# Optimization experiments

Hardware: AMD Instinct MI355X
Metric: run time of the kernel (lower is better)

Reference implementation:

```python
import jax, jax.numpy as jnp
import numpy as np

DIM = 1536
NUM_HEADS = 12
HEAD_DIM = DIM // NUM_HEADS  # 128
EPS = 1e-6


def _rms_norm(x, weight, eps=EPS):
    # x: [B, S, C], computed in float32 like the torch module
    xf = x.astype(jnp.float32)
    xf = xf * jax.lax.rsqrt(jnp.mean(xf * xf, axis=-1, keepdims=True) + eps)
    return (xf * weight).astype(x.dtype)


def _rotate_half(x):
    x1, x2 = jnp.split(x, 2, axis=-1)
    return jnp.concatenate([-x2, x1], axis=-1)


def setup_inputs() -> dict:
    key = jax.random.key(0)
    ks = jax.random.split(key, 12)
    B, S = 1, 4096
    scale = 1.0 / np.sqrt(DIM)
    x = jax.random.normal(ks[0], (B, S, DIM), dtype=jnp.float32)
    # RoPE tables [S, head_dim]
    pos = jnp.arange(S, dtype=jnp.float32)[:, None]
    inv_freq = 1.0 / (10000.0 ** (jnp.arange(0, HEAD_DIM, 2, dtype=jnp.float32) / HEAD_DIM))
    ang = pos * inv_freq[None, :]                      # [S, head_dim/2]
    ang = jnp.concatenate([ang, ang], axis=-1)         # [S, head_dim]
    freqs_cos = jnp.cos(ang)
    freqs_sin = jnp.sin(ang)
    Wq = jax.random.normal(ks[1], (DIM, DIM), dtype=jnp.float32) * scale
    bq = jnp.zeros((DIM,), dtype=jnp.float32)
    Wk = jax.random.normal(ks[2], (DIM, DIM), dtype=jnp.float32) * scale
    bk = jnp.zeros((DIM,), dtype=jnp.float32)
    Wv = jax.random.normal(ks[3], (DIM, DIM), dtype=jnp.float32) * scale
    bv = jnp.zeros((DIM,), dtype=jnp.float32)
    Wo = jax.random.normal(ks[4], (DIM, DIM), dtype=jnp.float32) * scale
    bo = jnp.zeros((DIM,), dtype=jnp.float32)
    gq = jnp.ones((DIM,), dtype=jnp.float32)
    gk = jnp.ones((DIM,), dtype=jnp.float32)
    return {"x": x, "freqs_cos": freqs_cos, "freqs_sin": freqs_sin,
            "Wq": Wq, "bq": bq, "Wk": Wk, "bk": bk, "Wv": Wv, "bv": bv,
            "Wo": Wo, "bo": bo, "gq": gq, "gk": gk}


def reference(x, freqs_cos, freqs_sin, Wq, bq, Wk, bk, Wv, bv, Wo, bo, gq, gk):
    b, s, _ = x.shape
    n, d = NUM_HEADS, HEAD_DIM
    q = _rms_norm(x @ Wq.T + bq, gq).reshape(b, s, n, d)
    k = _rms_norm(x @ Wk.T + bk, gk).reshape(b, s, n, d)
    v = (x @ Wv.T + bv).reshape(b, s, n, d)
    # RoPE: freqs [S, d] -> broadcast over batch and heads
    cos = freqs_cos[None, :, None, :]
    sin = freqs_sin[None, :, None, :]
    q = q * cos + _rotate_half(q) * sin
    k = k * cos + _rotate_half(k) * sin
    # SDPA, non-causal
    scores = jnp.einsum('bqnd,bknd->bnqk', q, k) / jnp.sqrt(jnp.asarray(d, x.dtype))
    attn = jax.nn.softmax(scores, axis=-1)
    out = jnp.einsum('bnqk,bknd->bqnd', attn, v).reshape(b, s, n * d)
    return out @ Wo.T + bo
```

## Files before the change

### kernel.cpp

```cpp
#include <hip/hip_runtime.h>

typedef unsigned short ushort_t;
typedef short bf16x8 __attribute__((ext_vector_type(8)));
typedef float f32x4 __attribute__((ext_vector_type(4)));
typedef float f32x16 __attribute__((ext_vector_type(16)));

#define S_LEN 4096
#define DIM   1536
#define NH    12
#define HD    128
#define KVSPLIT 4
#define ROWS (NH * S_LEN)
#define OPSPLIT_ELEMS ((size_t)ROWS * HD)

__device__ __forceinline__ float bf2f(ushort_t h) {
  union { unsigned u; float f; } v; v.u = ((unsigned)h) << 16; return v.f;
}
__device__ __forceinline__ ushort_t f2bf(float f) {
  union { float f; unsigned u; } v; v.f = f;
  return (ushort_t)((v.u + 0x7FFFu + ((v.u >> 16) & 1u)) >> 16);
}
__device__ __forceinline__ unsigned cvtpk(float lo, float hi_) {
  unsigned r; asm("v_cvt_pk_bf16_f32 %0, %1, %2" : "=v"(r) : "v"(lo), "v"(hi_)); return r;
}

#define GLD16(gp, lp) __builtin_amdgcn_global_load_lds( \
    (const __attribute__((address_space(1))) unsigned int*)(gp), \
    (__attribute__((address_space(3))) unsigned int*)(lp), 16, 0, 0)

__global__ void __launch_bounds__(256) cvt_bf16(const float* __restrict__ in,
                                                ushort_t* __restrict__ out, int n4) {
  int i = blockIdx.x * 256 + threadIdx.x;
  int stride = gridDim.x * 256;
  for (; i < n4; i += stride) {
    float4 v = ((const float4*)in)[i];
    ushort4 o;
    o.x = f2bf(v.x); o.y = f2bf(v.y); o.z = f2bf(v.z); o.w = f2bf(v.w);
    ((ushort4*)out)[i] = o;
  }
}

template <int F32OUT>
__global__ void __launch_bounds__(256) gemm_bt(
    const ushort_t* __restrict__ A, const ushort_t* __restrict__ Wbase,
    const float* __restrict__ b0, const float* __restrict__ b1, const float* __restrict__ b2,
    void* __restrict__ Cbase_v, int M, int N, int K)
{
  const int z = blockIdx.z;
  const ushort_t* W = Wbase + (size_t)z * N * K;
  const float* bias = (z == 0) ? b0 : (z == 1) ? b1 : b2;

  const int n0 = blockIdx.x * 128;
  const int m0 = blockIdx.y * 128;
  const int t = threadIdx.x;
  const int lane = t & 63;
  const int w = t >> 6;
  const int wr = w >> 1, wc = w & 1;
  const int mp = lane & 15, g = lane >> 4;

  __shared__ __attribute__((aligned(16))) ushort_t As[128 * 64];
  __shared__ __attribute__((aligned(16))) ushort_t Bs[128 * 64];

  f32x4 acc[4][4];
  f32x4 zero = {0.f, 0.f, 0.f, 0.f};
#pragma unroll
  for (int i = 0; i < 4; ++i)
#pragma unroll
    for (int j = 0; j < 4; ++j) acc[i][j] = zero;

  for (int kt = 0; kt < K; kt += 64) {
    __syncthreads();
#pragma unroll
    for (int i = 0; i < 4; ++i) {
      int p = i * 256 + t;
      int r = p >> 3, sl = p & 7;
      int sg = sl ^ (r & 7);
      GLD16(A + (size_t)(m0 + r) * K + kt + sg * 8, As + p * 8);
      GLD16(W + (size_t)(n0 + r) * K + kt + sg * 8, Bs + p * 8);
    }
    __syncthreads();
#pragma unroll
    for (int kk = 0; kk < 2; ++kk) {
      bf16x8 af[4], bfr[4];
#pragma unroll
      for (int mi = 0; mi < 4; ++mi) {
        int row = wr * 64 + mi * 16 + mp;
        int ch = (g + 4 * kk) ^ (row & 7);
        af[mi] = *(const bf16x8*)(As + row * 64 + ch * 8);
      }
#pragma unroll
      for (int ni = 0; ni < 4; ++ni) {
        int row = wc * 64 + ni * 16 + mp;
        int ch = (g + 4 * kk) ^ (row & 7);
        bfr[ni] = *(const bf16x8*)(Bs + row * 64 + ch * 8);
      }
#pragma unroll
      for (int mi = 0; mi < 4; ++mi)
#pragma unroll
        for (int ni = 0; ni < 4; ++ni)
          acc[mi][ni] = __builtin_amdgcn_mfma_f32_16x16x32_bf16(af[mi], bfr[ni], acc[mi][ni], 0, 0, 0);
    }
  }
#pragma unroll
  for (int ni = 0; ni < 4; ++ni) {
    int n = n0 + wc * 64 + ni * 16 + mp;
    float bv = bias[n];
#pragma unroll
    for (int mi = 0; mi < 4; ++mi) {
      int mbase = m0 + wr * 64 + mi * 16 + g * 4;
#pragma unroll
      for (int j = 0; j < 4; ++j) {
        if constexpr (F32OUT) {
          ((float*)Cbase_v)[(size_t)z * M * N + (size_t)(mbase + j) * N + n] =
              acc[mi][ni][j] + bv;
        } else {
          ((ushort_t*)Cbase_v)[(size_t)z * M * N + (size_t)(mbase + j) * N + n] =
              f2bf(acc[mi][ni][j] + bv);
        }
      }
    }
  }
}

__global__ void __launch_bounds__(256) epi_qkv(
    const ushort_t* __restrict__ raw,
    const float* __restrict__ gq, const float* __restrict__ gk,
    const float* __restrict__ fcos, const float* __restrict__ fsin,
    ushort_t* __restrict__ Qh, ushort_t* __restrict__ Kh, ushort_t* __restrict__ Vh)
{
  const int s = blockIdx.x;
  const int t = threadIdx.x;
  const ushort_t* rq = raw + (size_t)s * DIM;
  const ushort_t* rk = raw + (size_t)S_LEN * DIM + (size_t)s * DIM;
  const ushort_t* rv = raw + 2 * (size_t)S_LEN * DIM + (size_t)s * DIM;

  float sq = 0.f, sk = 0.f;
#pragma unroll
  for (int i = 0; i < 6; ++i) {
    int e = t + 256 * i;
    float a = bf2f(rq[e]); sq += a * a;
    float b = bf2f(rk[e]); sk += b * b;
  }
  for (int off = 1; off < 64; off <<= 1) {
    sq += __shfl_xor(sq, off, 64);
    sk += __shfl_xor(sk, off, 64);
  }
  __shared__ float red[2][4];
  int w = t >> 6;
  if ((t & 63) == 0) { red[0][w] = sq; red[1][w] = sk; }
  __syncthreads();
  sq = red[0][0] + red[0][1] + red[0][2] + red[0][3];
  sk = red[1][0] + red[1][1] + red[1][2] + red[1][3];
  float invq = rsqrtf(sq * (1.f / 1536.f) + 1e-6f);
  float invk = rsqrtf(sk * (1.f / 1536.f) + 1e-6f);

  const float qscale = 0.12752004708465604f;
#pragma unroll
  for (int i = 0; i < 3; ++i) {
    int p = t + 256 * i;
    int hh = p >> 6, d = p & 63;
    int e1 = hh * 128 + d, e2 = e1 + 64;
    float c1 = fcos[s * 128 + d],      s1 = fsin[s * 128 + d];
    float c2 = fcos[s * 128 + d + 64], s2 = fsin[s * 128 + d + 64];
    float q1 = bf2f(rq[e1]) * invq * gq[e1];
    float q2 = bf2f(rq[e2]) * invq * gq[e2];
    float k1 = bf2f(rk[e1]) * invk * gk[e1];
    float k2 = bf2f(rk[e2]) * invk * gk[e2];
    size_t ob = ((size_t)hh * S_LEN + s) * 128;
    Qh[ob + d]      = f2bf((q1 * c1 - q2 * s1) * qscale);
    Qh[ob + d + 64] = f2bf((q2 * c2 + q1 * s2) * qscale);
    Kh[ob + d]      = f2bf(k1 * c1 - k2 * s1);
    Kh[ob + d + 64] = f2bf(k2 * c2 + k1 * s2);
  }
#pragma unroll
  for (int i = 0; i < 6; ++i) {
    int e = t + 256 * i;
    int hh = e >> 7, d = e & 127;
    Vh[((size_t)hh * S_LEN + s) * 128 + d] = rv[e];
  }
}

__global__ void __launch_bounds__(256) transpose_v(const ushort_t* __restrict__ Vh,
                                                   ushort_t* __restrict__ VT) {
  const int st = blockIdx.x * 64;
  const int dt = blockIdx.y * 64;
  const int h = blockIdx.z;
  __shared__ ushort_t tile[64][65];
  const int t = threadIdx.x;
#pragma unroll
  for (int i = 0; i < 2; ++i) {
    int p = i * 256 + t;
    int r = p >> 3, c = (p & 7) * 8;
    bf16x8 v = *(const bf16x8*)(Vh + ((size_t)h * S_LEN + st + r) * 128 + dt + c);
#pragma unroll
    for (int j = 0; j < 8; ++j) tile[r][c + j] = ((ushort_t*)&v)[j];
  }
  __syncthreads();
#pragma unroll
  for (int i = 0; i < 2; ++i) {
    int p = i * 256 + t;
    int r = p >> 3, c = (p & 7) * 8;
    ushort_t tmp[8];
#pragma unroll
    for (int j = 0; j < 8; ++j) tmp[j] = tile[c + j][r];
    *(bf16x8*)(VT + ((size_t)h * 128 + dt + r) * S_LEN + st + c) = *(bf16x8*)tmp;
  }
}

__global__ void __launch_bounds__(128) attn32(
    const ushort_t* __restrict__ Qh, const ushort_t* __restrict__ Kh,
    const ushort_t* __restrict__ VT,
    ushort_t* __restrict__ opraw, ushort_t* __restrict__ opxb,
    float* __restrict__ mlbuf)
{
  const int qt = blockIdx.x;
  const int h = blockIdx.y;
  const int z = blockIdx.z;
  const int t = threadIdx.x;
  const int lane = t & 63;
  const int w = t >> 6;
  const int ql = lane & 31;
  const int hi = lane >> 5;

  __shared__ __attribute__((aligned(16))) ushort_t Ks[64 * 128];
  __shared__ __attribute__((aligned(16))) ushort_t Vs[128 * 64];

  const int q0 = qt * 64 + w * 32;
  const size_t kbase = (size_t)h * S_LEN * 128;
  const size_t vbase = (size_t)h * 128 * S_LEN;

  bf16x8 qf[8];
#pragma unroll
  for (int s = 0; s < 8; ++s)
    qf[s] = *(const bf16x8*)(Qh + ((size_t)h * S_LEN + q0 + ql) * 128 + 16 * s + 8 * hi);

  f32x16 oacc[4];
#pragma unroll
  for (int dt = 0; dt < 4; ++dt)
#pragma unroll
    for (int r = 0; r < 16; ++r) oacc[dt][r] = 0.f;
  float mrun = -1e30f, lrun = 0.f;

  const int kvbeg = z * (S_LEN / KVSPLIT);
  const int kvend = kvbeg + S_LEN / KVSPLIT;
  for (int kv0 = kvbeg; kv0 < kvend; kv0 += 64) {
    __syncthreads();
#pragma unroll
    for (int i = 0; i < 8; ++i) {
      int p = i * 128 + t;
      int r = p >> 4, sl = p & 15;
      int sg = sl ^ (r & 7);
      GLD16(Kh + kbase + (size_t)(kv0 + r) * 128 + sg * 8, Ks + p * 8);
    }
#pragma unroll
    for (int i = 0; i < 8; ++i) {
      int p = i * 128 + t;
      int r = p >> 3, sl = p & 7;
      int sg = sl ^ (r & 7);
      GLD16(VT + vbase + (size_t)r * S_LEN + kv0 + sg * 8, Vs + p * 8);
    }
    __syncthreads();

    f32x16 sa0, sa1;
#pragma unroll
    for (int r = 0; r < 16; ++r) { sa0[r] = 0.f; sa1[r] = 0.f; }
    __builtin_amdgcn_s_setprio(1);
#pragma unroll
    for (int s = 0; s < 8; ++s) {
      int ck = (2 * s + hi) ^ (ql & 7);
      bf16x8 k0 = *(const bf16x8*)(Ks + ql * 128 + ck * 8);
      bf16x8 k1 = *(const bf16x8*)(Ks + (32 + ql) * 128 + ck * 8);
      sa0 = __builtin_amdgcn_mfma_f32_32x32x16_bf16(k0, qf[s], sa0, 0, 0, 0);
      sa1 = __builtin_amdgcn_mfma_f32_32x32x16_bf16(k1, qf[s], sa1, 0, 0, 0);
    }
    __builtin_amdgcn_s_setprio(0);

    float mt[8];
#pragma unroll
    for (int r = 0; r < 8; ++r)
      mt[r] = fmaxf(fmaxf(sa0[r], sa0[r + 8]), fmaxf(sa1[r], sa1[r + 8]));
#pragma unroll
    for (int off = 4; off > 0; off >>= 1)
#pragma unroll
      for (int r = 0; r < 8; ++r)
        if (r < off) mt[r] = fmaxf(mt[r], mt[r + off]);
    float mx = fmaxf(mt[0], __shfl_xor(mt[0], 32));

    if (__any(mx - mrun > 11.0f)) {
      float nm = fmaxf(mrun, mx);
      float sc = exp2f(mrun - nm);
      mrun = nm;
      lrun *= sc;
#pragma unroll
      for (int dt = 0; dt < 4; ++dt)
#pragma unroll
        for (int r = 0; r < 16; ++r) oacc[dt][r] *= sc;
    }

    float rt[8];
#pragma unroll
    for (int r = 0; r < 16; ++r) {
      sa0[r] = exp2f(sa0[r] - mrun);
      sa1[r] = exp2f(sa1[r] - mrun);
    }
#pragma unroll
    for (int r = 0; r < 8; ++r) rt[r] = (sa0[r] + sa0[r + 8]) + (sa1[r] + sa1[r + 8]);
#pragma unroll
    for (int off = 4; off > 0; off >>= 1)
#pragma unroll
      for (int r = 0; r < 8; ++r)
        if (r < off) rt[r] += rt[r + off];
    lrun += rt[0] + __shfl_xor(rt[0], 32);

    unsigned pw0[8], pw1[8];
#pragma unroll
    for (int a = 0; a < 4; ++a) {
      pw0[2 * a]     = cvtpk(sa0[4 * a], sa0[4 * a + 1]);
      pw0[2 * a + 1] = cvtpk(sa0[4 * a + 2], sa0[4 * a + 3]);
      pw1[2 * a]     = cvtpk(sa1[4 * a], sa1[4 * a + 1]);
      pw1[2 * a + 1] = cvtpk(sa1[4 * a + 2], sa1[4 * a + 3]);
    }

#pragma unroll
    for (int st = 0; st < 2; ++st) {
#pragma unroll
      for (int ks = 0; ks < 2; ++ks) {
        unsigned q0w0 = st ? pw1[4 * ks + 0] : pw0[4 * ks + 0];
        unsigned q0w1 = st ? pw1[4 * ks + 1] : pw0[4 * ks + 1];
        unsigned q1w0 = st ? pw1[4 * ks + 2] : pw0[4 * ks + 2];
        unsigned q1w1 = st ? pw1[4 * ks + 3] : pw0[4 * ks + 3];
        unsigned sw0 = hi ? q0w0 : q1w0;
        unsigned sw1 = hi ? q0w1 : q1w1;
        unsigned rv0 = (unsigned)__shfl_xor((int)sw0, 32);
        unsigned rv1 = (unsigned)__shfl_xor((int)sw1, 32);
        union { unsigned u[4]; bf16x8 v; } fw;
        fw.u[0] = hi ? rv0 : q0w0;
        fw.u[1] = hi ? rv1 : q0w1;
        fw.u[2] = hi ? q1w0 : rv0;
        fw.u[3] = hi ? q1w1 : rv1;
        __builtin_amdgcn_s_setprio(1);
#pragma unroll
        for (int dt = 0; dt < 4; ++dt) {
          int d = 32 * dt + ql;
          int cv = (4 * st + 2 * ks + hi) ^ (ql & 7);
          bf16x8 va = *(const bf16x8*)(Vs + d * 64 + cv * 8);
          oacc[dt] = __builtin_amdgcn_mfma_f32_32x32x16_bf16(va, fw.v, oacc[dt], 0, 0, 0);
        }
        __builtin_amdgcn_s_setprio(0);
      }
    }
  }

  ushort_t* Op = (z < 3) ? (opraw + (size_t)z * OPSPLIT_ELEMS) : opxb;
  const int row = h * S_LEN + q0 + ql;
  float inv = 1.f / lrun;
#pragma unroll
  for (int dt = 0; dt < 4; ++dt) {
#pragma unroll
    for (int c = 0; c < 4; ++c) {
      float f0 = oacc[dt][4 * c + 0] * inv, f1 = oacc[dt][4 * c + 1] * inv;
      float f2 = oacc[dt][4 * c + 2] * inv, f3 = oacc[dt][4 * c + 3] * inv;
      uint2 u;
      u.x = cvtpk(f0, f1);
      u.y = cvtpk(f2, f3);
      *(uint2*)(Op + (size_t)row * 128 + 32 * dt + 8 * c + 4 * hi) = u;
    }
  }
  if (hi == 0) {
    mlbuf[2 * ((size_t)z * ROWS + row)]     = mrun;
    mlbuf[2 * ((size_t)z * ROWS + row) + 1] = lrun;
  }
}

__global__ void __launch_bounds__(256) attn_combine(
    const ushort_t* __restrict__ opraw, const ushort_t* __restrict__ opxb,
    const float* __restrict__ mlbuf, ushort_t* __restrict__ hb)
{
  int gidx = blockIdx.x * 256 + threadIdx.x;
  int r = gidx >> 4;
  int c = gidx & 15;

  float m[KVSPLIT], l[KVSPLIT];
#pragma unroll
  for (int zz = 0; zz < KVSPLIT; ++zz) {
    m[zz] = mlbuf[2 * ((size_t)zz * ROWS + r)];
    l[zz] = mlbuf[2 * ((size_t)zz * ROWS + r) + 1];
  }
  float M = fmaxf(fmaxf(m[0], m[1]), fmaxf(m[2], m[3]));
  float wsum = 0.f, wz[KVSPLIT];
#pragma unroll
  for (int zz = 0; zz < KVSPLIT; ++zz) {
    wz[zz] = l[zz] * exp2f(m[zz] - M);
    wsum += wz[zz];
  }
  float invw = 1.f / wsum;

  float o[8];
#pragma unroll
  for (int j = 0; j < 8; ++j) o[j] = 0.f;
#pragma unroll
  for (int zz = 0; zz < KVSPLIT; ++zz) {
    const ushort_t* Op = (zz < 3) ? (opraw + (size_t)zz * OPSPLIT_ELEMS) : opxb;
    bf16x8 v = *(const bf16x8*)(Op + (size_t)r * 128 + c * 8);
#pragma unroll
    for (int j = 0; j < 8; ++j) o[j] += wz[zz] * bf2f((ushort_t)v[j]);
  }
  uint4 u;
  u.x = cvtpk(o[0] * invw, o[1] * invw);
  u.y = cvtpk(o[2] * invw, o[3] * invw);
  u.z = cvtpk(o[4] * invw, o[5] * invw);
  u.w = cvtpk(o[6] * invw, o[7] * invw);
  int q = r & (S_LEN - 1), h = r >> 12;
  *(uint4*)(hb + (size_t)q * DIM + h * 128 + c * 8) = u;
}

extern "C" void kernel_launch(void* const* d_in, const int* in_sizes, int n_in,
                              void* d_out, int out_size, void* d_ws, size_t ws_size,
                              hipStream_t stream) {
  const float* x    = (const float*)d_in[0];
  const float* fcos = (const float*)d_in[1];
  const float* fsin = (const float*)d_in[2];
  const float* Wq   = (const float*)d_in[3];
  const float* bq   = (const float*)d_in[4];
  const float* Wk   = (const float*)d_in[5];
  const float* bk   = (const float*)d_in[6];
  const float* Wv   = (const float*)d_in[7];
  const float* bv   = (const float*)d_in[8];
  const float* Wo   = (const float*)d_in[9];
  const float* bo   = (const float*)d_in[10];
  const float* gq   = (const float*)d_in[11];
  const float* gk   = (const float*)d_in[12];

  char* ws = (char*)d_ws;
  ushort_t* xb  = (ushort_t*)(ws);
  ushort_t* wb  = (ushort_t*)(ws + 12582912);
  ushort_t* raw = (ushort_t*)(ws + 31457280);
  ushort_t* Qh  = (ushort_t*)(ws + 69206016);
  ushort_t* Kh  = (ushort_t*)(ws + 81788928);
  ushort_t* Vh  = (ushort_t*)(ws + 94371840);
  ushort_t* VT  = (ushort_t*)(ws + 106954752);
  ushort_t* hb  = (ushort_t*)(ws + 119537664);

  cvt_bf16<<<2048, 256, 0, stream>>>(x,  xb,             6291456 / 4);
  cvt_bf16<<<2048, 256, 0, stream>>>(Wq, wb + 0 * 2359296, 2359296 / 4);
  cvt_bf16<<<2048, 256, 0, stream>>>(Wk, wb + 1 * 2359296, 2359296 / 4);
  cvt_bf16<<<2048, 256, 0, stream>>>(Wv, wb + 2 * 2359296, 2359296 / 4);
  cvt_bf16<<<2048, 256, 0, stream>>>(Wo, wb + 3 * 2359296, 2359296 / 4);

  gemm_bt<0><<<dim3(12, 32, 3), 256, 0, stream>>>(xb, wb, bq, bk, bv,
                                                  (void*)raw, 4096, 1536, 1536);
  epi_qkv<<<4096, 256, 0, stream>>>(raw, gq, gk, fcos, fsin, Qh, Kh, Vh);
  transpose_v<<<dim3(64, 2, 12), 256, 0, stream>>>(Vh, VT);
  attn32<<<dim3(64, 12, KVSPLIT), 128, 0, stream>>>(Qh, Kh, VT, raw, xb, (float*)Vh);
  attn_combine<<<3072, 256, 0, stream>>>(raw, xb, (const float*)Vh, hb);
  gemm_bt<1><<<dim3(12, 32, 1), 256, 0, stream>>>(hb, wb + 3 * 2359296, bo, bo, bo,
                                                  (void*)d_out, 4096, 1536, 1536);
}
```

Measured before the change: 529.7 us.

## Add double-buffered KV staging attention kernel for half the KV splits

```diff
diff --git a/kernel.cpp b/kernel.cpp
--- a/kernel.cpp
+++ b/kernel.cpp
@@ -207,15 +207,156 @@
   }
 }
 
+__device__ __forceinline__ void stage_kv(const ushort_t* __restrict__ Kg,
+                                         const ushort_t* __restrict__ Vg,
+                                         ushort_t* KsB, ushort_t* VsB, int t) {
+#pragma unroll
+  for (int i = 0; i < 8; ++i) {
+    int p = i * 128 + t;
+    int r = p >> 4, sl = p & 15;
+    int sg = sl ^ (r & 7);
+    GLD16(Kg + (size_t)r * 128 + sg * 8, KsB + p * 8);
+  }
+#pragma unroll
+  for (int i = 0; i < 8; ++i) {
+    int p = i * 128 + t;
+    int r = p >> 3, sl = p & 7;
+    int sg = sl ^ (r & 7);
+    GLD16(Vg + (size_t)r * S_LEN + sg * 8, VsB + p * 8);
+  }
+}
+
+struct AttnState {
+  f32x16 oacc[4];
+  float mrun, lrun;
+};
+
+__device__ __forceinline__ void attn_tile(const ushort_t* KsB, const ushort_t* VsB,
+                                          const bf16x8* qf, AttnState& st_,
+                                          int ql, int hi) {
+  f32x16 sa0, sa1;
+#pragma unroll
+  for (int r = 0; r < 16; ++r) { sa0[r] = 0.f; sa1[r] = 0.f; }
+  __builtin_amdgcn_s_setprio(1);
+#pragma unroll
+  for (int s = 0; s < 8; ++s) {
+    int ck = (2 * s + hi) ^ (ql & 7);
+    bf16x8 k0 = *(const bf16x8*)(KsB + ql * 128 + ck * 8);
+    bf16x8 k1 = *(const bf16x8*)(KsB + (32 + ql) * 128 + ck * 8);
+    sa0 = __builtin_amdgcn_mfma_f32_32x32x16_bf16(k0, qf[s], sa0, 0, 0, 0);
+    sa1 = __builtin_amdgcn_mfma_f32_32x32x16_bf16(k1, qf[s], sa1, 0, 0, 0);
+  }
+  __builtin_amdgcn_s_setprio(0);
+
+  float mt[8];
+#pragma unroll
+  for (int r = 0; r < 8; ++r)
+    mt[r] = fmaxf(fmaxf(sa0[r], sa0[r + 8]), fmaxf(sa1[r], sa1[r + 8]));
+#pragma unroll
+  for (int off = 4; off > 0; off >>= 1)
+#pragma unroll
+    for (int r = 0; r < 8; ++r)
+      if (r < off) mt[r] = fmaxf(mt[r], mt[r + off]);
+  float mx = fmaxf(mt[0], __shfl_xor(mt[0], 32));
+
+  if (__any(mx - st_.mrun > 11.0f)) {
+    float nm = fmaxf(st_.mrun, mx);
+    float sc = exp2f(st_.mrun - nm);
+    st_.mrun = nm;
+    st_.lrun *= sc;
+#pragma unroll
+    for (int dt = 0; dt < 4; ++dt)
+#pragma unroll
+      for (int r = 0; r < 16; ++r) st_.oacc[dt][r] *= sc;
+  }
+
+  float rt[8];
+#pragma unroll
+  for (int r = 0; r < 16; ++r) {
+    sa0[r] = exp2f(sa0[r] - st_.mrun);
+    sa1[r] = exp2f(sa1[r] - st_.mrun);
+  }
+#pragma unroll
+  for (int r = 0; r < 8; ++r) rt[r] = (sa0[r] + sa0[r + 8]) + (sa1[r] + sa1[r + 8]);
+#pragma unroll
+  for (int off = 4; off > 0; off >>= 1)
+#pragma unroll
+    for (int r = 0; r < 8; ++r)
+      if (r < off) rt[r] += rt[r + off];
+  st_.lrun += rt[0] + __shfl_xor(rt[0], 32);
+
+  unsigned pw0[8], pw1[8];
+#pragma unroll
+  for (int a = 0; a < 4; ++a) {
+    pw0[2 * a]     = cvtpk(sa0[4 * a], sa0[4 * a + 1]);
+    pw0[2 * a + 1] = cvtpk(sa0[4 * a + 2], sa0[4 * a + 3]);
+    pw1[2 * a]     = cvtpk(sa1[4 * a], sa1[4 * a + 1]);
+    pw1[2 * a + 1] = cvtpk(sa1[4 * a + 2], sa1[4 * a + 3]);
+  }
+
+#pragma unroll
+  for (int sx = 0; sx < 2; ++sx) {
+#pragma unroll
+    for (int ks = 0; ks < 2; ++ks) {
+      unsigned q0w0 = sx ? pw1[4 * ks + 0] : pw0[4 * ks + 0];
+      unsigned q0w1 = sx ? pw1[4 * ks + 1] : pw0[4 * ks + 1];
+      unsigned q1w0 = sx ? pw1[4 * ks + 2] : pw0[4 * ks + 2];
+      unsigned q1w1 = sx ? pw1[4 * ks + 3] : pw0[4 * ks + 3];
+      unsigned sw0 = hi ? q0w0 : q1w0;
+      unsigned sw1 = hi ? q0w1 : q1w1;
+      unsigned rv0 = (unsigned)__shfl_xor((int)sw0, 32);
+      unsigned rv1 = (unsigned)__shfl_xor((int)sw1, 32);
+      union { unsigned u[4]; bf16x8 v; } fw;
+      fw.u[0] = hi ? rv0 : q0w0;
+      fw.u[1] = hi ? rv1 : q0w1;
+      fw.u[2] = hi ? q1w0 : rv0;
+      fw.u[3] = hi ? q1w1 : rv1;
+      __builtin_amdgcn_s_setprio(1);
+#pragma unroll
+      for (int dt = 0; dt < 4; ++dt) {
+        int d = 32 * dt + ql;
+        int cv = (4 * sx + 2 * ks + hi) ^ (ql & 7);
+        bf16x8 va = *(const bf16x8*)(VsB + d * 64 + cv * 8);
+        st_.oacc[dt] = __builtin_amdgcn_mfma_f32_32x32x16_bf16(va, fw.v, st_.oacc[dt], 0, 0, 0);
+      }
+      __builtin_amdgcn_s_setprio(0);
+    }
+  }
+}
+
+__device__ __forceinline__ void attn_epilogue(AttnState& st_, int z, int row, int hi,
+                                              ushort_t* __restrict__ opraw,
+                                              ushort_t* __restrict__ opxb,
+                                              float* __restrict__ mlbuf) {
+  ushort_t* Op = (z < 3) ? (opraw + (size_t)z * OPSPLIT_ELEMS) : opxb;
+  float inv = 1.f / st_.lrun;
+#pragma unroll
+  for (int dt = 0; dt < 4; ++dt) {
+#pragma unroll
+    for (int c = 0; c < 4; ++c) {
+      float f0 = st_.oacc[dt][4 * c + 0] * inv, f1 = st_.oacc[dt][4 * c + 1] * inv;
+      float f2 = st_.oacc[dt][4 * c + 2] * inv, f3 = st_.oacc[dt][4 * c + 3] * inv;
+      uint2 u;
+      u.x = cvtpk(f0, f1);
+      u.y = cvtpk(f2, f3);
+      *(uint2*)(Op + (size_t)row * 128 + 32 * dt + 8 * c + 4 * hi) = u;
+    }
+  }
+  if (hi == 0) {
+    mlbuf[2 * ((size_t)z * ROWS + row)]     = st_.mrun;
+    mlbuf[2 * ((size_t)z * ROWS + row) + 1] = st_.lrun;
+  }
+}
+
 __global__ void __launch_bounds__(128) attn32(
     const ushort_t* __restrict__ Qh, const ushort_t* __restrict__ Kh,
     const ushort_t* __restrict__ VT,
     ushort_t* __restrict__ opraw, ushort_t* __restrict__ opxb,
-    float* __restrict__ mlbuf)
+    float* __restrict__ mlbuf, int zoff)
 {
   const int qt = blockIdx.x;
   const int h = blockIdx.y;
-  const int z = blockIdx.z;
+  const int z = blockIdx.z + zoff;
   const int t = threadIdx.x;
   const int lane = t & 63;
   const int w = t >> 6;
@@ -234,142 +375,79 @@
   for (int s = 0; s < 8; ++s)
     qf[s] = *(const bf16x8*)(Qh + ((size_t)h * S_LEN + q0 + ql) * 128 + 16 * s + 8 * hi);
 
-  f32x16 oacc[4];
+  AttnState st_;
 #pragma unroll
   for (int dt = 0; dt < 4; ++dt)
 #pragma unroll
-    for (int r = 0; r < 16; ++r) oacc[dt][r] = 0.f;
-  float mrun = -1e30f, lrun = 0.f;
+    for (int r = 0; r < 16; ++r) st_.oacc[dt][r] = 0.f;
+  st_.mrun = -1e30f; st_.lrun = 0.f;
 
   const int kvbeg = z * (S_LEN / KVSPLIT);
   const int kvend = kvbeg + S_LEN / KVSPLIT;
   for (int kv0 = kvbeg; kv0 < kvend; kv0 += 64) {
     __syncthreads();
-#pragma unroll
-    for (int i = 0; i < 8; ++i) {
-      int p = i * 128 + t;
-      int r = p >> 4, sl = p & 15;
-      int sg = sl ^ (r & 7);
-      GLD16(Kh + kbase + (size_t)(kv0 + r) * 128 + sg * 8, Ks + p * 8);
+    stage_kv(Kh + kbase + (size_t)kv0 * 128, VT + vbase + kv0, Ks, Vs, t);
+    __syncthreads();
+    attn_tile(Ks, Vs, qf, st_, ql, hi);
+  }
+  attn_epilogue(st_, z, h * S_LEN + q0 + ql, hi, opraw, opxb, mlbuf);
+}
+
+__global__ void __launch_bounds__(128) attn32p(
+    const ushort_t* __restrict__ Qh, const ushort_t* __restrict__ Kh,
+    const ushort_t* __restrict__ VT,
+    ushort_t* __restrict__ opraw, ushort_t* __restrict__ opxb,
+    float* __restrict__ mlbuf, int zoff)
+{
+  const int qt = blockIdx.x;
+  const int h = blockIdx.y;
+  const int z = blockIdx.z + zoff;
+  const int t = threadIdx.x;
+  const int lane = t & 63;
+  const int w = t >> 6;
+  const int ql = lane & 31;
+  const int hi = lane >> 5;
+
+  __shared__ __attribute__((aligned(16))) ushort_t Ks[2][64 * 128];
+  __shared__ __attribute__((aligned(16))) ushort_t Vs[2][128 * 64];
+
+  const int q0 = qt * 64 + w * 32;
+  const size_t kbase = (size_t)h * S_LEN * 128;
+  const size_t vbase = (size_t)h * 128 * S_LEN;
+
+  bf16x8 qf[8];
+#pragma unroll
+  for (int s = 0; s < 8; ++s)
+    qf[s] = *(const bf16x8*)(Qh + ((size_t)h * S_LEN + q0 + ql) * 128 + 16 * s + 8 * hi);
+
+  AttnState st_;
+#pragma unroll
+  for (int dt = 0; dt < 4; ++dt)
+#pragma unroll
+    for (int r = 0; r < 16; ++r) st_.oacc[dt][r] = 0.f;
+  st_.mrun = -1e30f; st_.lrun = 0.f;
+
+  const int kvbeg = z * (S_LEN / KVSPLIT);
+  const int NT = (S_LEN / KVSPLIT) / 64;
+
+  stage_kv(Kh + kbase + (size_t)kvbeg * 128, VT + vbase + kvbeg, Ks[0], Vs[0], t);
+
+  for (int it = 0; it < NT; ++it) {
+    const int cur = it & 1;
+    if (it + 1 < NT) {
+      const int kvn = kvbeg + (it + 1) * 64;
+      stage_kv(Kh + kbase + (size_t)kvn * 128, VT + vbase + kvn, Ks[cur ^ 1], Vs[cur ^ 1], t);
+      asm volatile("s_waitcnt vmcnt(16)" ::: "memory");
+    } else {
+      asm volatile("s_waitcnt vmcnt(0)" ::: "memory");
     }
-#pragma unroll
-    for (int i = 0; i < 8; ++i) {
-      int p = i * 128 + t;
-      int r = p >> 3, sl = p & 7;
-      int sg = sl ^ (r & 7);
-      GLD16(VT + vbase + (size_t)r * S_LEN + kv0 + sg * 8, Vs + p * 8);
-    }
-    __syncthreads();
-
-    f32x16 sa0, sa1;
-#pragma unroll
-    for (int r = 0; r < 16; ++r) { sa0[r] = 0.f; sa1[r] = 0.f; }
-    __builtin_amdgcn_s_setprio(1);
-#pragma unroll
-    for (int s = 0; s < 8; ++s) {
-      int ck = (2 * s + hi) ^ (ql & 7);
-      bf16x8 k0 = *(const bf16x8*)(Ks + ql * 128 + ck * 8);
-      bf16x8 k1 = *(const bf16x8*)(Ks + (32 + ql) * 128 + ck * 8);
-      sa0 = __builtin_amdgcn_mfma_f32_32x32x16_bf16(k0, qf[s], sa0, 0, 0, 0);
-      sa1 = __builtin_amdgcn_mfma_f32_32x32x16_bf16(k1, qf[s], sa1, 0, 0, 0);
-    }
-    __builtin_amdgcn_s_setprio(0);
-
-    float mt[8];
-#pragma unroll
-    for (int r = 0; r < 8; ++r)
-      mt[r] = fmaxf(fmaxf(sa0[r], sa0[r + 8]), fmaxf(sa1[r], sa1[r + 8]));
-#pragma unroll
-    for (int off = 4; off > 0; off >>= 1)
-#pragma unroll
-      for (int r = 0; r < 8; ++r)
-        if (r < off) mt[r] = fmaxf(mt[r], mt[r + off]);
-    float mx = fmaxf(mt[0], __shfl_xor(mt[0], 32));
-
-    if (__any(mx - mrun > 11.0f)) {
-      float nm = fmaxf(mrun, mx);
-      float sc = exp2f(mrun - nm);
-      mrun = nm;
-      lrun *= sc;
-#pragma unroll
-      for (int dt = 0; dt < 4; ++dt)
-#pragma unroll
-        for (int r = 0; r < 16; ++r) oacc[dt][r] *= sc;
-    }
-
-    float rt[8];
-#pragma unroll
-    for (int r = 0; r < 16; ++r) {
-      sa0[r] = exp2f(sa0[r] - mrun);
-      sa1[r] = exp2f(sa1[r] - mrun);
-    }
-#pragma unroll
-    for (int r = 0; r < 8; ++r) rt[r] = (sa0[r] + sa0[r + 8]) + (sa1[r] + sa1[r + 8]);
-#pragma unroll
-    for (int off = 4; off > 0; off >>= 1)
-#pragma unroll
-      for (int r = 0; r < 8; ++r)
-        if (r < off) rt[r] += rt[r + off];
-    lrun += rt[0] + __shfl_xor(rt[0], 32);
-
-    unsigned pw0[8], pw1[8];
-#pragma unroll
-    for (int a = 0; a < 4; ++a) {
-      pw0[2 * a]     = cvtpk(sa0[4 * a], sa0[4 * a + 1]);
-      pw0[2 * a + 1] = cvtpk(sa0[4 * a + 2], sa0[4 * a + 3]);
-      pw1[2 * a]     = cvtpk(sa1[4 * a], sa1[4 * a + 1]);
-      pw1[2 * a + 1] = cvtpk(sa1[4 * a + 2], sa1[4 * a + 3]);
-    }
-
-#pragma unroll
-    for (int st = 0; st < 2; ++st) {
-#pragma unroll
-      for (int ks = 0; ks < 2; ++ks) {
-        unsigned q0w0 = st ? pw1[4 * ks + 0] : pw0[4 * ks + 0];
-        unsigned q0w1 = st ? pw1[4 * ks + 1] : pw0[4 * ks + 1];
-        unsigned q1w0 = st ? pw1[4 * ks + 2] : pw0[4 * ks + 2];
-        unsigned q1w1 = st ? pw1[4 * ks + 3] : pw0[4 * ks + 3];
-        unsigned sw0 = hi ? q0w0 : q1w0;
-        unsigned sw1 = hi ? q0w1 : q1w1;
-        unsigned rv0 = (unsigned)__shfl_xor((int)sw0, 32);
-        unsigned rv1 = (unsigned)__shfl_xor((int)sw1, 32);
-        union { unsigned u[4]; bf16x8 v; } fw;
-        fw.u[0] = hi ? rv0 : q0w0;
-        fw.u[1] = hi ? rv1 : q0w1;
-        fw.u[2] = hi ? q1w0 : rv0;
-        fw.u[3] = hi ? q1w1 : rv1;
-        __builtin_amdgcn_s_setprio(1);
-#pragma unroll
-        for (int dt = 0; dt < 4; ++dt) {
-          int d = 32 * dt + ql;
-          int cv = (4 * st + 2 * ks + hi) ^ (ql & 7);
-          bf16x8 va = *(const bf16x8*)(Vs + d * 64 + cv * 8);
-          oacc[dt] = __builtin_amdgcn_mfma_f32_32x32x16_bf16(va, fw.v, oacc[dt], 0, 0, 0);
-        }
-        __builtin_amdgcn_s_setprio(0);
-      }
-    }
-  }
-
-  ushort_t* Op = (z < 3) ? (opraw + (size_t)z * OPSPLIT_ELEMS) : opxb;
-  const int row = h * S_LEN + q0 + ql;
-  float inv = 1.f / lrun;
-#pragma unroll
-  for (int dt = 0; dt < 4; ++dt) {
-#pragma unroll
-    for (int c = 0; c < 4; ++c) {
-      float f0 = oacc[dt][4 * c + 0] * inv, f1 = oacc[dt][4 * c + 1] * inv;
-      float f2 = oacc[dt][4 * c + 2] * inv, f3 = oacc[dt][4 * c + 3] * inv;
-      uint2 u;
-      u.x = cvtpk(f0, f1);
-      u.y = cvtpk(f2, f3);
-      *(uint2*)(Op + (size_t)row * 128 + 32 * dt + 8 * c + 4 * hi) = u;
-    }
-  }
-  if (hi == 0) {
-    mlbuf[2 * ((size_t)z * ROWS + row)]     = mrun;
-    mlbuf[2 * ((size_t)z * ROWS + row) + 1] = lrun;
-  }
+    __builtin_amdgcn_sched_barrier(0);
+    __builtin_amdgcn_s_barrier();
+    __builtin_amdgcn_sched_barrier(0);
+    attn_tile(Ks[cur], Vs[cur], qf, st_, ql, hi);
+    __builtin_amdgcn_s_barrier();
+  }
+  attn_epilogue(st_, z, h * S_LEN + q0 + ql, hi, opraw, opxb, mlbuf);
 }
 
 __global__ void __launch_bounds__(256) attn_combine(
@@ -451,7 +529,10 @@
                                                   (void*)raw, 4096, 1536, 1536);
   epi_qkv<<<4096, 256, 0, stream>>>(raw, gq, gk, fcos, fsin, Qh, Kh, Vh);
   transpose_v<<<dim3(64, 2, 12), 256, 0, stream>>>(Vh, VT);
-  attn32<<<dim3(64, 12, KVSPLIT), 128, 0, stream>>>(Qh, Kh, VT, raw, xb, (float*)Vh);
+
+  attn32 <<<dim3(64, 12, 2), 128, 0, stream>>>(Qh, Kh, VT, raw, xb, (float*)Vh, 0);
+  attn32p<<<dim3(64, 12, 2), 128, 0, stream>>>(Qh, Kh, VT, raw, xb, (float*)Vh, 2);
+
   attn_combine<<<3072, 256, 0, stream>>>(raw, xb, (const float*)Vh, hb);
   gemm_bt<1><<<dim3(12, 32, 1), 256, 0, stream>>>(hb, wb + 3 * 2359296, bo, bo, bo,
                                                   (void*)d_out, 4096, 1536, 1536);
```

New measurement: 536.0 us. About the same (+1.2%).
